# Performance work log

Measured on AMD Instinct MI355X. Metric: run time of the kernel, lower is better.

Reference implementation:

```python
import jax, jax.numpy as jnp
import numpy as np

N, NUM_CLASSES, FEAT_DIM = 32768, 395, 512


def setup_inputs() -> dict:
    key = jax.random.key(0)
    k1, k2, k3, k4 = jax.random.split(key, 4)
    modal1_inputs = jax.random.normal(k1, (N, FEAT_DIM), dtype=jnp.float32)
    modal2_inputs = jax.random.normal(k2, (N, FEAT_DIM), dtype=jnp.float32)
    targets = jax.random.randint(k3, (N,), 0, NUM_CLASSES)
    # learned centers parameter: torch.rand -> uniform [0, 1)
    centers = jax.random.uniform(k4, (NUM_CLASSES, FEAT_DIM), dtype=jnp.float32)
    return {
        "modal1_inputs": modal1_inputs,
        "modal2_inputs": modal2_inputs,
        "centers": centers,
        "targets": targets,
    }


def _smooth_l1(a, b):
    # SmoothL1Loss with default beta=1.0, reduction='mean'
    d = jnp.abs(a - b)
    return jnp.mean(jnp.where(d < 1.0, 0.5 * d * d, d - 0.5))


def reference(modal1_inputs, modal2_inputs, centers, targets):
    num_classes = centers.shape[0]
    # Per-label mean (the original O(N^2) loop is exactly a segment mean
    # gathered back per sample).
    ones = jnp.ones((targets.shape[0],), dtype=modal1_inputs.dtype)
    counts = jax.ops.segment_sum(ones, targets, num_segments=num_classes)
    counts = jnp.maximum(counts, 1.0)  # empty classes never gathered
    sum1 = jax.ops.segment_sum(modal1_inputs, targets, num_segments=num_classes)
    sum2 = jax.ops.segment_sum(modal2_inputs, targets, num_segments=num_classes)
    centersR = (sum1 / counts[:, None])[targets]  # [N, D]
    centersT = (sum2 / counts[:, None])[targets]  # [N, D]
    gathered_centers = centers[targets]           # [N, D]
    loss = _smooth_l1(centersR, gathered_centers) + _smooth_l1(centersT, gathered_centers)
    return loss
```

## Files before the change

kernel.cpp:

```cpp
#include <hip/hip_runtime.h>

#define NS 32768
#define NC 395
#define FD 512
#define SPL 16
#define CHUNK (NS / SPL)
#define TPB 256

__device__ float g_partial[SPL * 2 * NC * FD];
__device__ int   g_pcount[SPL * NC];

__device__ __forceinline__ void f4add(float4& a, const float4 b) {
    a.x += b.x; a.y += b.y; a.z += b.z; a.w += b.w;
}

__global__ __launch_bounds__(TPB)
void gather_sum_kernel(const float4* __restrict__ m1,
                       const float4* __restrict__ m2,
                       const int* __restrict__ targets,
                       float* __restrict__ out) {
    int c   = blockIdx.x >> 4;
    int s   = blockIdx.x & (SPL - 1);
    int tid = threadIdx.x;

    if (blockIdx.x == 0 && tid == 0) out[0] = 0.0f;

    __shared__ int sidx[CHUNK];
    __shared__ int scnt;
    if (tid == 0) scnt = 0;
    __syncthreads();

    int sbase = s * CHUNK;
    const int4* t4 = reinterpret_cast<const int4*>(targets + sbase);
    int4 ta = t4[tid];
    int4 tb = t4[tid + TPB];
    int i0 = sbase + 4 * tid;
    int i1 = sbase + 4 * (tid + TPB);
    if (ta.x == c) sidx[atomicAdd(&scnt, 1)] = i0;
    if (ta.y == c) sidx[atomicAdd(&scnt, 1)] = i0 + 1;
    if (ta.z == c) sidx[atomicAdd(&scnt, 1)] = i0 + 2;
    if (ta.w == c) sidx[atomicAdd(&scnt, 1)] = i0 + 3;
    if (tb.x == c) sidx[atomicAdd(&scnt, 1)] = i1;
    if (tb.y == c) sidx[atomicAdd(&scnt, 1)] = i1 + 1;
    if (tb.z == c) sidx[atomicAdd(&scnt, 1)] = i1 + 2;
    if (tb.w == c) sidx[atomicAdd(&scnt, 1)] = i1 + 3;
    __syncthreads();
    int cnt = scnt;

    int m = tid >> 7;
    int q = tid & 127;
    const float4* src = m ? m2 : m1;

    float4 a0 = make_float4(0.f, 0.f, 0.f, 0.f);
    float4 a1 = a0, a2 = a0, a3 = a0;

    int j = 0;
    for (; j + 4 <= cnt; j += 4) {
        int s0 = sidx[j], s1 = sidx[j + 1], s2 = sidx[j + 2], s3 = sidx[j + 3];
        float4 v0 = src[(size_t)s0 * 128 + q];
        float4 v1 = src[(size_t)s1 * 128 + q];
        float4 v2 = src[(size_t)s2 * 128 + q];
        float4 v3 = src[(size_t)s3 * 128 + q];
        f4add(a0, v0); f4add(a1, v1); f4add(a2, v2); f4add(a3, v3);
    }
    for (; j < cnt; j++)
        f4add(a0, src[(size_t)sidx[j] * 128 + q]);
    f4add(a0, a1); f4add(a2, a3); f4add(a0, a2);

    float4* dst = reinterpret_cast<float4*>(g_partial);
    dst[(((size_t)s * 2 + m) * NC + c) * 128 + q] = a0;
    if (tid == 0) g_pcount[s * NC + c] = cnt;
}

__device__ __forceinline__ float smooth_l1(float d) {
    d = fabsf(d);
    return d < 1.0f ? 0.5f * d * d : d - 0.5f;
}

__global__ void loss_kernel(const float* __restrict__ centers,
                            float* __restrict__ out) {
    __shared__ float scnt[NC];
    int t = threadIdx.x;
    for (int c = t; c < NC; c += 256) {
        int sc = 0;
        #pragma unroll
        for (int k = 0; k < SPL; k++) sc += g_pcount[k * NC + c];
        scnt[c] = (float)sc;
    }
    __syncthreads();

    float val = 0.0f;
    for (int gid = blockIdx.x * 256 + t; gid < NC * FD; gid += gridDim.x * 256) {
        int c = gid >> 9;
        float cnt = scnt[c];
        if (cnt > 0.0f) {
            float sum1 = 0.0f, sum2 = 0.0f;
            #pragma unroll
            for (int k = 0; k < SPL; k++) {
                sum1 += g_partial[(size_t)(2 * k)     * NC * FD + gid];
                sum2 += g_partial[(size_t)(2 * k + 1) * NC * FD + gid];
            }
            float ctr = centers[gid];
            float inv = 1.0f / cnt;
            val += cnt * (smooth_l1(sum1 * inv - ctr) + smooth_l1(sum2 * inv - ctr));
        }
    }

    for (int off = 32; off > 0; off >>= 1)
        val += __shfl_down(val, off, 64);
    __shared__ float wsum[4];
    int lane = t & 63, wid = t >> 6;
    if (lane == 0) wsum[wid] = val;
    __syncthreads();
    if (t == 0) {
        float sm = wsum[0] + wsum[1] + wsum[2] + wsum[3];
        atomicAdd(out, sm * 5.9604644775390625e-08f);
    }
}

extern "C" void kernel_launch(void* const* d_in, const int* in_sizes, int n_in,
                              void* d_out, int out_size, void* d_ws, size_t ws_size,
                              hipStream_t stream) {
    const float4* m1 = (const float4*)d_in[0];
    const float4* m2 = (const float4*)d_in[1];
    const float* centers = (const float*)d_in[2];
    const int* targets = (const int*)d_in[3];
    float* out = (float*)d_out;

    gather_sum_kernel<<<NC * SPL, TPB, 0, stream>>>(m1, m2, targets, out);
    loss_kernel<<<512, 256, 0, stream>>>(centers, out);
}
```

Before: 173.7 us.

## Fuse gather-sum and loss into one kernel with atomic grid barrier

Merges the segment-sum and loss kernels into a single launch. Every block increments a global done counter, and the first 256 blocks spin until all blocks have finished, then reduce the partials into the loss. The split factor is halved to 8, which halves partial storage and reduction reads but gives each block a longer gather loop, now unrolled by 8. The spin barrier depends on all 3160 blocks being able to make progress; otherwise waiting blocks could deadlock. The two memsets added to the launch also cost time.

```diff
diff --git a/kernel.cpp b/kernel.cpp
--- a/kernel.cpp
+++ b/kernel.cpp
@@ -3,9 +3,13 @@
 #define NS 32768
 #define NC 395
 #define FD 512
-#define SPL 16
+#define SPL 8
 #define CHUNK (NS / SPL)
 #define TPB 256
+#define GRID (NC * SPL)
+#define RED 256
+#define NEL (NC * FD)
+#define PER (NEL / RED)
 
 __device__ float g_partial[SPL * 2 * NC * FD];
 __device__ int   g_pcount[SPL * NC];
@@ -13,17 +17,21 @@
 __device__ __forceinline__ void f4add(float4& a, const float4 b) {
     a.x += b.x; a.y += b.y; a.z += b.z; a.w += b.w;
 }
+__device__ __forceinline__ float smooth_l1(float d) {
+    d = fabsf(d);
+    return d < 1.0f ? 0.5f * d * d : d - 0.5f;
+}
 
 __global__ __launch_bounds__(TPB)
-void gather_sum_kernel(const float4* __restrict__ m1,
-                       const float4* __restrict__ m2,
-                       const int* __restrict__ targets,
-                       float* __restrict__ out) {
-    int c   = blockIdx.x >> 4;
+void fused_kernel(const float4* __restrict__ m1,
+                  const float4* __restrict__ m2,
+                  const int* __restrict__ targets,
+                  const float* __restrict__ centers,
+                  float* __restrict__ out,
+                  int* __restrict__ done) {
+    int c   = blockIdx.x >> 3;
     int s   = blockIdx.x & (SPL - 1);
     int tid = threadIdx.x;
-
-    if (blockIdx.x == 0 && tid == 0) out[0] = 0.0f;
 
     __shared__ int sidx[CHUNK];
     __shared__ int scnt;
@@ -34,8 +42,12 @@
     const int4* t4 = reinterpret_cast<const int4*>(targets + sbase);
     int4 ta = t4[tid];
     int4 tb = t4[tid + TPB];
+    int4 tc = t4[tid + 2 * TPB];
+    int4 td = t4[tid + 3 * TPB];
     int i0 = sbase + 4 * tid;
     int i1 = sbase + 4 * (tid + TPB);
+    int i2 = sbase + 4 * (tid + 2 * TPB);
+    int i3 = sbase + 4 * (tid + 3 * TPB);
     if (ta.x == c) sidx[atomicAdd(&scnt, 1)] = i0;
     if (ta.y == c) sidx[atomicAdd(&scnt, 1)] = i0 + 1;
     if (ta.z == c) sidx[atomicAdd(&scnt, 1)] = i0 + 2;
@@ -44,6 +56,14 @@
     if (tb.y == c) sidx[atomicAdd(&scnt, 1)] = i1 + 1;
     if (tb.z == c) sidx[atomicAdd(&scnt, 1)] = i1 + 2;
     if (tb.w == c) sidx[atomicAdd(&scnt, 1)] = i1 + 3;
+    if (tc.x == c) sidx[atomicAdd(&scnt, 1)] = i2;
+    if (tc.y == c) sidx[atomicAdd(&scnt, 1)] = i2 + 1;
+    if (tc.z == c) sidx[atomicAdd(&scnt, 1)] = i2 + 2;
+    if (tc.w == c) sidx[atomicAdd(&scnt, 1)] = i2 + 3;
+    if (td.x == c) sidx[atomicAdd(&scnt, 1)] = i3;
+    if (td.y == c) sidx[atomicAdd(&scnt, 1)] = i3 + 1;
+    if (td.z == c) sidx[atomicAdd(&scnt, 1)] = i3 + 2;
+    if (td.w == c) sidx[atomicAdd(&scnt, 1)] = i3 + 3;
     __syncthreads();
     int cnt = scnt;
 
@@ -55,12 +75,23 @@
     float4 a1 = a0, a2 = a0, a3 = a0;
 
     int j = 0;
+    for (; j + 8 <= cnt; j += 8) {
+        float4 v0 = src[(size_t)sidx[j]     * 128 + q];
+        float4 v1 = src[(size_t)sidx[j + 1] * 128 + q];
+        float4 v2 = src[(size_t)sidx[j + 2] * 128 + q];
+        float4 v3 = src[(size_t)sidx[j + 3] * 128 + q];
+        float4 v4 = src[(size_t)sidx[j + 4] * 128 + q];
+        float4 v5 = src[(size_t)sidx[j + 5] * 128 + q];
+        float4 v6 = src[(size_t)sidx[j + 6] * 128 + q];
+        float4 v7 = src[(size_t)sidx[j + 7] * 128 + q];
+        f4add(a0, v0); f4add(a1, v1); f4add(a2, v2); f4add(a3, v3);
+        f4add(a0, v4); f4add(a1, v5); f4add(a2, v6); f4add(a3, v7);
+    }
     for (; j + 4 <= cnt; j += 4) {
-        int s0 = sidx[j], s1 = sidx[j + 1], s2 = sidx[j + 2], s3 = sidx[j + 3];
-        float4 v0 = src[(size_t)s0 * 128 + q];
-        float4 v1 = src[(size_t)s1 * 128 + q];
-        float4 v2 = src[(size_t)s2 * 128 + q];
-        float4 v3 = src[(size_t)s3 * 128 + q];
+        float4 v0 = src[(size_t)sidx[j]     * 128 + q];
+        float4 v1 = src[(size_t)sidx[j + 1] * 128 + q];
+        float4 v2 = src[(size_t)sidx[j + 2] * 128 + q];
+        float4 v3 = src[(size_t)sidx[j + 3] * 128 + q];
         f4add(a0, v0); f4add(a1, v1); f4add(a2, v2); f4add(a3, v3);
     }
     for (; j < cnt; j++)
@@ -70,49 +101,48 @@
     float4* dst = reinterpret_cast<float4*>(g_partial);
     dst[(((size_t)s * 2 + m) * NC + c) * 128 + q] = a0;
     if (tid == 0) g_pcount[s * NC + c] = cnt;
-}
 
-__device__ __forceinline__ float smooth_l1(float d) {
-    d = fabsf(d);
-    return d < 1.0f ? 0.5f * d * d : d - 0.5f;
-}
+    __syncthreads();
+    if (tid == 0)
+        __hip_atomic_fetch_add(done, 1, __ATOMIC_RELEASE, __HIP_MEMORY_SCOPE_AGENT);
 
-__global__ void loss_kernel(const float* __restrict__ centers,
-                            float* __restrict__ out) {
-    __shared__ float scnt[NC];
-    int t = threadIdx.x;
-    for (int c = t; c < NC; c += 256) {
-        int sc = 0;
-        #pragma unroll
-        for (int k = 0; k < SPL; k++) sc += g_pcount[k * NC + c];
-        scnt[c] = (float)sc;
+    if (blockIdx.x >= RED) return;
+
+    if (tid == 0) {
+        while (__hip_atomic_load(done, __ATOMIC_ACQUIRE, __HIP_MEMORY_SCOPE_AGENT) < GRID)
+            __builtin_amdgcn_s_sleep(32);
     }
     __syncthreads();
 
     float val = 0.0f;
-    for (int gid = blockIdx.x * 256 + t; gid < NC * FD; gid += gridDim.x * 256) {
-        int c = gid >> 9;
-        float cnt = scnt[c];
-        if (cnt > 0.0f) {
-            float sum1 = 0.0f, sum2 = 0.0f;
+    int ebase = blockIdx.x * PER;
+    for (int e = tid; e < PER; e += TPB) {
+        int gid = ebase + e;
+        int cc = gid >> 9;
+        int icnt = 0;
+        #pragma unroll
+        for (int k = 0; k < SPL; k++) icnt += g_pcount[k * NC + cc];
+        if (icnt > 0) {
+            float s1 = 0.0f, s2 = 0.0f;
             #pragma unroll
             for (int k = 0; k < SPL; k++) {
-                sum1 += g_partial[(size_t)(2 * k)     * NC * FD + gid];
-                sum2 += g_partial[(size_t)(2 * k + 1) * NC * FD + gid];
+                s1 += g_partial[(size_t)(2 * k)     * NEL + gid];
+                s2 += g_partial[(size_t)(2 * k + 1) * NEL + gid];
             }
+            float fc = (float)icnt;
             float ctr = centers[gid];
-            float inv = 1.0f / cnt;
-            val += cnt * (smooth_l1(sum1 * inv - ctr) + smooth_l1(sum2 * inv - ctr));
+            float inv = 1.0f / fc;
+            val += fc * (smooth_l1(s1 * inv - ctr) + smooth_l1(s2 * inv - ctr));
         }
     }
 
     for (int off = 32; off > 0; off >>= 1)
         val += __shfl_down(val, off, 64);
     __shared__ float wsum[4];
-    int lane = t & 63, wid = t >> 6;
+    int lane = tid & 63, wid = tid >> 6;
     if (lane == 0) wsum[wid] = val;
     __syncthreads();
-    if (t == 0) {
+    if (tid == 0) {
         float sm = wsum[0] + wsum[1] + wsum[2] + wsum[3];
         atomicAdd(out, sm * 5.9604644775390625e-08f);
     }
@@ -126,7 +156,9 @@
     const float* centers = (const float*)d_in[2];
     const int* targets = (const int*)d_in[3];
     float* out = (float*)d_out;
+    int* done = (int*)d_ws;
 
-    gather_sum_kernel<<<NC * SPL, TPB, 0, stream>>>(m1, m2, targets, out);
-    loss_kernel<<<512, 256, 0, stream>>>(centers, out);
+    hipMemsetAsync(done, 0, sizeof(int), stream);
+    hipMemsetAsync(out, 0, sizeof(float), stream);
+    fused_kernel<<<GRID, TPB, 0, stream>>>(m1, m2, targets, centers, out, done);
 }
```

Result: slower. 407.2 us (+134.4%).

## Halve sample splits and split gather across wave pairs with LDS combine

Applied to the files above, without the earlier changes.

Reduces the number of sample chunks per class from 16 to 8, so each block scans twice as many targets and the partial-sum buffer and the loss kernel's reduction shrink by half. Within a block, each modality now uses two waves that take alternating sample indices, and each lane accumulates two float4 columns. The two waves' results are combined through shared memory before writing. The intent is to cut the redundant target scanning across the 6320 blocks and the partial-buffer traffic, at the cost of half as many blocks and a longer per-block scan.

```diff
diff --git a/kernel.cpp b/kernel.cpp
--- a/kernel.cpp
+++ b/kernel.cpp
@@ -3,9 +3,10 @@
 #define NS 32768
 #define NC 395
 #define FD 512
-#define SPL 16
+#define SPL 8
 #define CHUNK (NS / SPL)
 #define TPB 256
+#define NEL (NC * FD)
 
 __device__ float g_partial[SPL * 2 * NC * FD];
 __device__ int   g_pcount[SPL * NC];
@@ -19,7 +20,7 @@
                        const float4* __restrict__ m2,
                        const int* __restrict__ targets,
                        float* __restrict__ out) {
-    int c   = blockIdx.x >> 4;
+    int c   = blockIdx.x >> 3;
     int s   = blockIdx.x & (SPL - 1);
     int tid = threadIdx.x;
 
@@ -27,15 +28,20 @@
 
     __shared__ int sidx[CHUNK];
     __shared__ int scnt;
-    if (tid == 0) scnt = 0;
-    __syncthreads();
+    __shared__ float4 cmb[2][128];
 
     int sbase = s * CHUNK;
     const int4* t4 = reinterpret_cast<const int4*>(targets + sbase);
     int4 ta = t4[tid];
     int4 tb = t4[tid + TPB];
+    int4 tc = t4[tid + 2 * TPB];
+    int4 td = t4[tid + 3 * TPB];
+    if (tid == 0) scnt = 0;
+    __syncthreads();
     int i0 = sbase + 4 * tid;
     int i1 = sbase + 4 * (tid + TPB);
+    int i2 = sbase + 4 * (tid + 2 * TPB);
+    int i3 = sbase + 4 * (tid + 3 * TPB);
     if (ta.x == c) sidx[atomicAdd(&scnt, 1)] = i0;
     if (ta.y == c) sidx[atomicAdd(&scnt, 1)] = i0 + 1;
     if (ta.z == c) sidx[atomicAdd(&scnt, 1)] = i0 + 2;
@@ -44,31 +50,60 @@
     if (tb.y == c) sidx[atomicAdd(&scnt, 1)] = i1 + 1;
     if (tb.z == c) sidx[atomicAdd(&scnt, 1)] = i1 + 2;
     if (tb.w == c) sidx[atomicAdd(&scnt, 1)] = i1 + 3;
+    if (tc.x == c) sidx[atomicAdd(&scnt, 1)] = i2;
+    if (tc.y == c) sidx[atomicAdd(&scnt, 1)] = i2 + 1;
+    if (tc.z == c) sidx[atomicAdd(&scnt, 1)] = i2 + 2;
+    if (tc.w == c) sidx[atomicAdd(&scnt, 1)] = i2 + 3;
+    if (td.x == c) sidx[atomicAdd(&scnt, 1)] = i3;
+    if (td.y == c) sidx[atomicAdd(&scnt, 1)] = i3 + 1;
+    if (td.z == c) sidx[atomicAdd(&scnt, 1)] = i3 + 2;
+    if (td.w == c) sidx[atomicAdd(&scnt, 1)] = i3 + 3;
     __syncthreads();
     int cnt = scnt;
 
-    int m = tid >> 7;
-    int q = tid & 127;
-    const float4* src = m ? m2 : m1;
+    int wid  = tid >> 6;
+    int mod  = wid >> 1;
+    int wsub = wid & 1;
+    int lane = tid & 63;
+    const float4* src = mod ? m2 : m1;
 
-    float4 a0 = make_float4(0.f, 0.f, 0.f, 0.f);
-    float4 a1 = a0, a2 = a0, a3 = a0;
+    float4 z = make_float4(0.f, 0.f, 0.f, 0.f);
+    float4 aA0 = z, aB0 = z, aA1 = z, aB1 = z;
 
-    int j = 0;
-    for (; j + 4 <= cnt; j += 4) {
-        int s0 = sidx[j], s1 = sidx[j + 1], s2 = sidx[j + 2], s3 = sidx[j + 3];
-        float4 v0 = src[(size_t)s0 * 128 + q];
-        float4 v1 = src[(size_t)s1 * 128 + q];
-        float4 v2 = src[(size_t)s2 * 128 + q];
-        float4 v3 = src[(size_t)s3 * 128 + q];
-        f4add(a0, v0); f4add(a1, v1); f4add(a2, v2); f4add(a3, v3);
+    int j = wsub;
+    for (; j + 6 < cnt; j += 8) {
+        const float4* p0 = src + (size_t)sidx[j]     * 128;
+        const float4* p1 = src + (size_t)sidx[j + 2] * 128;
+        const float4* p2 = src + (size_t)sidx[j + 4] * 128;
+        const float4* p3 = src + (size_t)sidx[j + 6] * 128;
+        float4 vA0 = p0[lane], vB0 = p0[lane + 64];
+        float4 vA1 = p1[lane], vB1 = p1[lane + 64];
+        float4 vA2 = p2[lane], vB2 = p2[lane + 64];
+        float4 vA3 = p3[lane], vB3 = p3[lane + 64];
+        f4add(aA0, vA0); f4add(aB0, vB0);
+        f4add(aA1, vA1); f4add(aB1, vB1);
+        f4add(aA0, vA2); f4add(aB0, vB2);
+        f4add(aA1, vA3); f4add(aB1, vB3);
     }
-    for (; j < cnt; j++)
-        f4add(a0, src[(size_t)sidx[j] * 128 + q]);
-    f4add(a0, a1); f4add(a2, a3); f4add(a0, a2);
+    for (; j < cnt; j += 2) {
+        const float4* p = src + (size_t)sidx[j] * 128;
+        f4add(aA0, p[lane]); f4add(aB0, p[lane + 64]);
+    }
+    f4add(aA0, aA1); f4add(aB0, aB1);
 
-    float4* dst = reinterpret_cast<float4*>(g_partial);
-    dst[(((size_t)s * 2 + m) * NC + c) * 128 + q] = a0;
+    if (wsub == 0) {
+        cmb[mod][lane]      = aA0;
+        cmb[mod][lane + 64] = aB0;
+    }
+    __syncthreads();
+    if (wsub == 1) {
+        float4 rA = cmb[mod][lane];      f4add(rA, aA0);
+        float4 rB = cmb[mod][lane + 64]; f4add(rB, aB0);
+        float4* dst = reinterpret_cast<float4*>(g_partial);
+        size_t base = (((size_t)s * 2 + mod) * NC + c) * 128;
+        dst[base + lane]      = rA;
+        dst[base + lane + 64] = rB;
+    }
     if (tid == 0) g_pcount[s * NC + c] = cnt;
 }
 
@@ -90,19 +125,19 @@
     __syncthreads();
 
     float val = 0.0f;
-    for (int gid = blockIdx.x * 256 + t; gid < NC * FD; gid += gridDim.x * 256) {
+    for (int gid = blockIdx.x * 256 + t; gid < NEL; gid += gridDim.x * 256) {
         int c = gid >> 9;
         float cnt = scnt[c];
         if (cnt > 0.0f) {
-            float sum1 = 0.0f, sum2 = 0.0f;
+            float s1 = 0.0f, s2 = 0.0f;
             #pragma unroll
             for (int k = 0; k < SPL; k++) {
-                sum1 += g_partial[(size_t)(2 * k)     * NC * FD + gid];
-                sum2 += g_partial[(size_t)(2 * k + 1) * NC * FD + gid];
+                s1 += g_partial[(size_t)(2 * k)     * NEL + gid];
+                s2 += g_partial[(size_t)(2 * k + 1) * NEL + gid];
             }
             float ctr = centers[gid];
             float inv = 1.0f / cnt;
-            val += cnt * (smooth_l1(sum1 * inv - ctr) + smooth_l1(sum2 * inv - ctr));
+            val += cnt * (smooth_l1(s1 * inv - ctr) + smooth_l1(s2 * inv - ctr));
         }
     }
 
```

After: 167.9 us. 3.3% less time.

## Split samples into 32 chunks with XCD-aware block mapping and 16-bit indices

Applied to the files above, without the earlier changes.

Doubles the number of sample chunks so each block scans 1024 targets instead of 2048. Blocks are remapped so that every block on a given XCD (assigned round-robin by blockIdx & 7) works on the same set of sample chunks, which keeps that XCD's input rows in its own L2. Shared index lists become 16-bit offsets relative to the chunk, and the gather loop is unrolled by 2 instead of 4. The cost is twice as many partial sums written to memory and read back in the loss kernel, plus less memory-level parallelism per thread in the gather.

```diff
diff --git a/kernel.cpp b/kernel.cpp
--- a/kernel.cpp
+++ b/kernel.cpp
@@ -3,9 +3,10 @@
 #define NS 32768
 #define NC 395
 #define FD 512
-#define SPL 16
+#define SPL 32
 #define CHUNK (NS / SPL)
 #define TPB 256
+#define NEL (NC * FD)
 
 __device__ float g_partial[SPL * 2 * NC * FD];
 __device__ int   g_pcount[SPL * NC];
@@ -19,56 +20,50 @@
                        const float4* __restrict__ m2,
                        const int* __restrict__ targets,
                        float* __restrict__ out) {
-    int c   = blockIdx.x >> 4;
-    int s   = blockIdx.x & (SPL - 1);
-    int tid = threadIdx.x;
+    int xcd  = blockIdx.x & 7;
+    int idx  = blockIdx.x >> 3;
+    int sgrp = idx / NC;
+    int c    = idx - sgrp * NC;
+    int s    = xcd + (sgrp << 3);
+    int tid  = threadIdx.x;
 
     if (blockIdx.x == 0 && tid == 0) out[0] = 0.0f;
 
-    __shared__ int sidx[CHUNK];
+    __shared__ unsigned short sidx[CHUNK];
     __shared__ int scnt;
-    if (tid == 0) scnt = 0;
-    __syncthreads();
 
     int sbase = s * CHUNK;
     const int4* t4 = reinterpret_cast<const int4*>(targets + sbase);
     int4 ta = t4[tid];
-    int4 tb = t4[tid + TPB];
-    int i0 = sbase + 4 * tid;
-    int i1 = sbase + 4 * (tid + TPB);
-    if (ta.x == c) sidx[atomicAdd(&scnt, 1)] = i0;
-    if (ta.y == c) sidx[atomicAdd(&scnt, 1)] = i0 + 1;
-    if (ta.z == c) sidx[atomicAdd(&scnt, 1)] = i0 + 2;
-    if (ta.w == c) sidx[atomicAdd(&scnt, 1)] = i0 + 3;
-    if (tb.x == c) sidx[atomicAdd(&scnt, 1)] = i1;
-    if (tb.y == c) sidx[atomicAdd(&scnt, 1)] = i1 + 1;
-    if (tb.z == c) sidx[atomicAdd(&scnt, 1)] = i1 + 2;
-    if (tb.w == c) sidx[atomicAdd(&scnt, 1)] = i1 + 3;
+    if (tid == 0) scnt = 0;
+    __syncthreads();
+    int i0 = 4 * tid;
+    if (ta.x == c) sidx[atomicAdd(&scnt, 1)] = (unsigned short)i0;
+    if (ta.y == c) sidx[atomicAdd(&scnt, 1)] = (unsigned short)(i0 + 1);
+    if (ta.z == c) sidx[atomicAdd(&scnt, 1)] = (unsigned short)(i0 + 2);
+    if (ta.w == c) sidx[atomicAdd(&scnt, 1)] = (unsigned short)(i0 + 3);
     __syncthreads();
     int cnt = scnt;
 
-    int m = tid >> 7;
-    int q = tid & 127;
-    const float4* src = m ? m2 : m1;
+    int mod = tid >> 7;
+    int q   = tid & 127;
+    const float4* src = (mod ? m2 : m1) + (size_t)sbase * 128;
 
     float4 a0 = make_float4(0.f, 0.f, 0.f, 0.f);
-    float4 a1 = a0, a2 = a0, a3 = a0;
+    float4 a1 = a0;
 
     int j = 0;
-    for (; j + 4 <= cnt; j += 4) {
-        int s0 = sidx[j], s1 = sidx[j + 1], s2 = sidx[j + 2], s3 = sidx[j + 3];
-        float4 v0 = src[(size_t)s0 * 128 + q];
-        float4 v1 = src[(size_t)s1 * 128 + q];
-        float4 v2 = src[(size_t)s2 * 128 + q];
-        float4 v3 = src[(size_t)s3 * 128 + q];
-        f4add(a0, v0); f4add(a1, v1); f4add(a2, v2); f4add(a3, v3);
+    for (; j + 2 <= cnt; j += 2) {
+        float4 v0 = src[(size_t)sidx[j]     * 128 + q];
+        float4 v1 = src[(size_t)sidx[j + 1] * 128 + q];
+        f4add(a0, v0); f4add(a1, v1);
     }
-    for (; j < cnt; j++)
+    if (j < cnt)
         f4add(a0, src[(size_t)sidx[j] * 128 + q]);
-    f4add(a0, a1); f4add(a2, a3); f4add(a0, a2);
+    f4add(a0, a1);
 
     float4* dst = reinterpret_cast<float4*>(g_partial);
-    dst[(((size_t)s * 2 + m) * NC + c) * 128 + q] = a0;
+    dst[(((size_t)s * 2 + mod) * NC + c) * 128 + q] = a0;
     if (tid == 0) g_pcount[s * NC + c] = cnt;
 }
 
@@ -83,26 +78,25 @@
     int t = threadIdx.x;
     for (int c = t; c < NC; c += 256) {
         int sc = 0;
-        #pragma unroll
         for (int k = 0; k < SPL; k++) sc += g_pcount[k * NC + c];
         scnt[c] = (float)sc;
     }
     __syncthreads();
 
     float val = 0.0f;
-    for (int gid = blockIdx.x * 256 + t; gid < NC * FD; gid += gridDim.x * 256) {
+    for (int gid = blockIdx.x * 256 + t; gid < NEL; gid += gridDim.x * 256) {
         int c = gid >> 9;
         float cnt = scnt[c];
         if (cnt > 0.0f) {
-            float sum1 = 0.0f, sum2 = 0.0f;
-            #pragma unroll
+            float s1 = 0.0f, s2 = 0.0f;
+            #pragma unroll 8
             for (int k = 0; k < SPL; k++) {
-                sum1 += g_partial[(size_t)(2 * k)     * NC * FD + gid];
-                sum2 += g_partial[(size_t)(2 * k + 1) * NC * FD + gid];
+                s1 += g_partial[(size_t)(2 * k)     * NEL + gid];
+                s2 += g_partial[(size_t)(2 * k + 1) * NEL + gid];
             }
             float ctr = centers[gid];
             float inv = 1.0f / cnt;
-            val += cnt * (smooth_l1(sum1 * inv - ctr) + smooth_l1(sum2 * inv - ctr));
+            val += cnt * (smooth_l1(s1 * inv - ctr) + smooth_l1(s2 * inv - ctr));
         }
     }
 
```

Result: slower. 178.0 us (+2.5%).
